# Kernel optimization log

Hardware: AMD Instinct MI355X
Metric: run time of the kernel (lower is better)

The kernel has to match this reference:

```python
import jax, jax.numpy as jnp
import numpy as np

N = 200000   # active voxels
K = 27       # 3x3x3 kernel volume
CIN = 32
COUT = 64


def setup_inputs() -> dict:
    key = jax.random.key(0)
    k1, k2, k3, k4 = jax.random.split(key, 4)
    features = jax.random.normal(k1, (N, CIN), dtype=jnp.float32)
    # kernel map: for each kernel offset k and output voxel n, index of the
    # contributing input voxel (or masked out if that neighbor is inactive)
    neighbor_map = jax.random.randint(k2, (K, N), 0, N, dtype=jnp.int32)
    neighbor_mask = jax.random.randint(k3, (K, N), 0, 2) > 0
    std = 1.0 / float(np.sqrt(CIN * K))  # matches reset_parameters
    kernel = jax.random.uniform(k4, (K, CIN, COUT), dtype=jnp.float32,
                                minval=-std, maxval=std)
    return {"features": features, "neighbor_map": neighbor_map,
            "neighbor_mask": neighbor_mask, "kernel": kernel}


def reference(features, neighbor_map, neighbor_mask, kernel):
    # Sparse conv3d as gather -> per-offset matmul -> accumulate.
    # scan over the K=27 kernel offsets keeps peak memory at one gathered
    # [N, CIN] buffer instead of materializing [K, N, CIN].
    n_out = features.shape[0]
    cout = kernel.shape[-1]

    def body(acc, inp):
        nm_k, mask_k, w_k = inp  # [N], [N], [CIN, COUT]
        g = features[nm_k] * mask_k[:, None].astype(features.dtype)  # gather [N, CIN]
        return acc + g @ w_k, None

    init = jnp.zeros((n_out, cout), dtype=features.dtype)
    out, _ = jax.lax.scan(body, init, (neighbor_map, neighbor_mask, kernel))
    return out
```

## Files before the change

### kernel.cpp

```cpp
#include <hip/hip_runtime.h>

#define CIN   32
#define COUT  64
#define K_OFF 27

typedef __attribute__((ext_vector_type(8))) short bf16x8;
typedef __attribute__((ext_vector_type(4))) float f32x4;

#define FENCE_VM(N) asm volatile("s_waitcnt vmcnt(" #N ")" ::: "memory")
#define PIN()       asm volatile("" ::: "memory")
#define BARRIER()   asm volatile("s_barrier" ::: "memory")

__device__ inline unsigned short f2bf_rne(float f) {
    union { float f; unsigned int u; } v; v.f = f;
    unsigned int u = v.u;
    u = (u + 0x7fffu + ((u >> 16) & 1u)) >> 16;
    return (unsigned short)u;
}

__device__ inline void async_load16(const void* g, void* l) {
    __builtin_amdgcn_global_load_lds(
        (const __attribute__((address_space(1))) void*)g,
        (__attribute__((address_space(3))) void*)l, 16, 0, 0);
}

__global__ __launch_bounds__(256) void prep_all(
    const float* __restrict__ feat, const int* __restrict__ nmap,
    const unsigned char* __restrict__ mask8, const float* __restrict__ wk,
    unsigned short* __restrict__ featb, int* __restrict__ midx,
    unsigned short* __restrict__ wt2, float* __restrict__ zrow,
    int n, int det_bytes)
{
    __shared__ int wany[4];
    const int tid = threadIdx.x;
    const int gsz = gridDim.x * 256;
    const int gt  = blockIdx.x * 256 + tid;

    {
        int found = 0;
        for (int i = tid; i < det_bytes; i += 256)
            if ((i & 3) && mask8[i]) found = 1;
        unsigned long long b = __ballot(found);
        if ((tid & 63) == 0) wany[tid >> 6] = b ? 1 : 0;
        __syncthreads();
    }
    const int is_b8 = wany[0] | wany[1] | wany[2] | wany[3];

    const int F = (n * CIN) / 8;
    for (int i = gt; i < F; i += gsz) {
        const int base = i * 8;
        float4 a = *(const float4*)(feat + base);
        float4 b = *(const float4*)(feat + base + 4);
        bf16x8 v;
        v[0] = (short)f2bf_rne(a.x); v[1] = (short)f2bf_rne(a.y);
        v[2] = (short)f2bf_rne(a.z); v[3] = (short)f2bf_rne(a.w);
        v[4] = (short)f2bf_rne(b.x); v[5] = (short)f2bf_rne(b.y);
        v[6] = (short)f2bf_rne(b.z); v[7] = (short)f2bf_rne(b.w);
        *(bf16x8*)(featb + base) = v;
    }

    {
        const int total = K_OFF * n;
        const int Q = (total + 3) / 4;
        for (int i = gt; i < Q; i += gsz) {
            int e = i * 4;
            if (e + 3 < total) {
                int4 nm = *(const int4*)(nmap + e);
                int m0, m1, m2, m3;
                if (is_b8) {
                    uchar4 mb = *(const uchar4*)(mask8 + e);
                    m0 = mb.x; m1 = mb.y; m2 = mb.z; m3 = mb.w;
                } else {
                    const int* m32 = (const int*)mask8;
                    int4 mm = *(const int4*)(m32 + e);
                    m0 = mm.x; m1 = mm.y; m2 = mm.z; m3 = mm.w;
                }
                int4 r;
                r.x = m0 ? nm.x : -1; r.y = m1 ? nm.y : -1;
                r.z = m2 ? nm.z : -1; r.w = m3 ? nm.w : -1;
                *(int4*)(midx + e) = r;
            } else {
                for (; e < total; ++e) {
                    int m = is_b8 ? (int)mask8[e] : ((const int*)mask8)[e];
                    midx[e] = m ? nmap[e] : -1;
                }
            }
        }
    }

    for (int t = gt; t < K_OFF * 4 * 64; t += gsz) {
        const int lane = t & 63, ct = (t >> 6) & 3, k = t >> 8;
        const int lrow = lane & 15, q = lane >> 4;
        const int col = ct * 16 + lrow;
        bf16x8 v;
        #pragma unroll
        for (int j = 0; j < 8; ++j)
            v[j] = (short)f2bf_rne(wk[(k * CIN + q * 8 + j) * COUT + col]);
        *(bf16x8*)(wt2 + t * 8) = v;
    }

    if (gt < 16) zrow[gt] = 0.0f;
}

__global__ __launch_bounds__(256) void conv_mfma10(
    const unsigned short* __restrict__ featb,
    const int*            __restrict__ midx,
    const unsigned short* __restrict__ wt2,
    const unsigned short* __restrict__ zrow,
    float* __restrict__ out, int n)
{
    __shared__ __attribute__((aligned(16))) unsigned short Bs[3][4][512];
    __shared__ __attribute__((aligned(16))) unsigned short As[3][4][2][512];

    const int tid  = threadIdx.x;
    const int wave = tid >> 6;
    const int lane = tid & 63;
    const int lrow = lane & 15;
    const int q    = lane >> 4;
    const int n0   = blockIdx.x * 128 + wave * 32;

    const int  row0 = n0 + lrow, row1 = n0 + 16 + lrow;
    const bool vr0 = row0 < n, vr1 = row1 < n;

    auto load_mi = [&](int k, int rt) -> int {
        const int  r = rt ? row1 : row0;
        const bool v = rt ? vr1 : vr0;
        if (!v) return -1;
        return midx[k * n + r];
    };
    auto issue_gather = [&](int mi, unsigned short* ldsbase) {
        const unsigned short* src =
            (mi >= 0) ? featb + (size_t)mi * CIN + q * 8 : zrow;
        async_load16(src, ldsbase);
    };
    auto stageB = [&](int k) {
        const unsigned short* src = wt2 + (((k * 4 + wave)) << 9) + lane * 8;
        async_load16(src, &Bs[k % 3][wave][0]);
    };

    int   mi_buf[2][2];
    f32x4 acc[2][4] = {};

    {
        int p00 = load_mi(0, 0), p01 = load_mi(0, 1);
        int p10 = load_mi(1, 0), p11 = load_mi(1, 1);
        mi_buf[0][0] = load_mi(2, 0); mi_buf[0][1] = load_mi(2, 1);
        mi_buf[1][0] = load_mi(3, 0); mi_buf[1][1] = load_mi(3, 1);
        PIN();
        stageB(0);
        stageB(1);
        PIN();
        issue_gather(p00, &As[0][wave][0][0]);
        issue_gather(p01, &As[0][wave][1][0]);
        PIN();
        issue_gather(p10, &As[1][wave][0][0]);
        issue_gather(p11, &As[1][wave][1][0]);
        PIN();
        FENCE_VM(2);
        BARRIER();
    }

    #pragma unroll
    for (int k = 0; k < K_OFF; ++k) {
        bf16x8 a0 = *(const bf16x8*)(&As[k % 3][wave][0][lane * 8]);
        bf16x8 a1 = *(const bf16x8*)(&As[k % 3][wave][1][lane * 8]);
        bf16x8 b0 = *(const bf16x8*)(&Bs[k % 3][0][lane * 8]);
        bf16x8 b1 = *(const bf16x8*)(&Bs[k % 3][1][lane * 8]);
        bf16x8 b2 = *(const bf16x8*)(&Bs[k % 3][2][lane * 8]);
        bf16x8 b3 = *(const bf16x8*)(&Bs[k % 3][3][lane * 8]);
        PIN();

        if (k + 2 < K_OFF) {
            stageB(k + 2);
            PIN();
            issue_gather(mi_buf[k & 1][0], &As[(k + 2) % 3][wave][0][0]);
            issue_gather(mi_buf[k & 1][1], &As[(k + 2) % 3][wave][1][0]);
            PIN();
        }
        if (k + 4 < K_OFF) {
            mi_buf[k & 1][0] = load_mi(k + 4, 0);
            mi_buf[k & 1][1] = load_mi(k + 4, 1);
            PIN();
        }

        acc[0][0] = __builtin_amdgcn_mfma_f32_16x16x32_bf16(a0, b0, acc[0][0], 0, 0, 0);
        acc[1][0] = __builtin_amdgcn_mfma_f32_16x16x32_bf16(a1, b0, acc[1][0], 0, 0, 0);
        acc[0][1] = __builtin_amdgcn_mfma_f32_16x16x32_bf16(a0, b1, acc[0][1], 0, 0, 0);
        acc[1][1] = __builtin_amdgcn_mfma_f32_16x16x32_bf16(a1, b1, acc[1][1], 0, 0, 0);
        acc[0][2] = __builtin_amdgcn_mfma_f32_16x16x32_bf16(a0, b2, acc[0][2], 0, 0, 0);
        acc[1][2] = __builtin_amdgcn_mfma_f32_16x16x32_bf16(a1, b2, acc[1][2], 0, 0, 0);
        acc[0][3] = __builtin_amdgcn_mfma_f32_16x16x32_bf16(a0, b3, acc[0][3], 0, 0, 0);
        acc[1][3] = __builtin_amdgcn_mfma_f32_16x16x32_bf16(a1, b3, acc[1][3], 0, 0, 0);

        if (k < K_OFF - 1) {
            if      (k == 0)  FENCE_VM(5);
            else if (k <= 22) FENCE_VM(7);
            else if (k == 23) FENCE_VM(5);
            else if (k == 24) FENCE_VM(3);
            else              FENCE_VM(0);
            BARRIER();
        }
    }

    #pragma unroll
    for (int rt = 0; rt < 2; ++rt)
        #pragma unroll
        for (int ct = 0; ct < 4; ++ct)
            #pragma unroll
            for (int r = 0; r < 4; ++r) {
                const int row = n0 + rt * 16 + q * 4 + r;
                if (row < n) out[(size_t)row * COUT + ct * 16 + lrow] = acc[rt][ct][r];
            }
}

__global__ __launch_bounds__(256) void detect_mask(
    const unsigned char* __restrict__ mask, int nbytes, int* __restrict__ flag,
    float* __restrict__ zrow) {
    __shared__ int wany[4];
    int found = 0;
    for (int i = threadIdx.x; i < nbytes; i += 256)
        if ((i & 3) && mask[i]) found = 1;
    unsigned long long b = __ballot(found);
    if ((threadIdx.x & 63) == 0) wany[threadIdx.x >> 6] = b ? 1 : 0;
    __syncthreads();
    if (threadIdx.x == 0) *flag = wany[0] | wany[1] | wany[2] | wany[3];
    if (threadIdx.x < 16) zrow[threadIdx.x] = 0.0f;
}

#define BN 64
__global__ __launch_bounds__(256) void sparse_conv_fp32(
    const float* __restrict__ feat, const int* __restrict__ nmap,
    const unsigned char* __restrict__ mask8, const int* __restrict__ mask32,
    const float* __restrict__ wk, float* __restrict__ out,
    int n, const int* __restrict__ flag)
{
    __shared__ float A[CIN][BN];
    __shared__ float W[CIN][COUT];
    const int tid = threadIdx.x;
    const int n0 = blockIdx.x * BN;
    const int is_b8 = *flag;
    const int r0 = (tid >> 4) * 4, c0 = (tid & 15) * 4;
    const int grow = tid >> 2, gpart = tid & 3;
    float acc[4][4] = {};
    for (int k = 0; k < K_OFF; ++k) {
        {
            const int base = tid * 8;
            const float* wsrc = wk + (size_t)k * (CIN * COUT) + base;
            float4 w0 = ((const float4*)wsrc)[0];
            float4 w1 = ((const float4*)wsrc)[1];
            *(float4*)&W[base >> 6][base & 63] = w0;
            *(float4*)&W[base >> 6][(base & 63) + 4] = w1;
        }
        {
            const int gn = n0 + grow;
            float4 f0 = make_float4(0.f, 0.f, 0.f, 0.f), f1 = f0;
            if (gn < n) {
                const int idx = k * n + gn;
                const int m = is_b8 ? (int)mask8[idx] : mask32[idx];
                if (m) {
                    const float* fsrc = feat + (size_t)nmap[idx] * CIN + gpart * 8;
                    f0 = ((const float4*)fsrc)[0];
                    f1 = ((const float4*)fsrc)[1];
                }
            }
            const int cb = gpart * 8;
            A[cb+0][grow]=f0.x; A[cb+1][grow]=f0.y; A[cb+2][grow]=f0.z; A[cb+3][grow]=f0.w;
            A[cb+4][grow]=f1.x; A[cb+5][grow]=f1.y; A[cb+6][grow]=f1.z; A[cb+7][grow]=f1.w;
        }
        __syncthreads();
        #pragma unroll
        for (int c = 0; c < CIN; ++c) {
            const float4 a = *(const float4*)&A[c][r0];
            const float4 w = *(const float4*)&W[c][c0];
            acc[0][0]+=a.x*w.x; acc[0][1]+=a.x*w.y; acc[0][2]+=a.x*w.z; acc[0][3]+=a.x*w.w;
            acc[1][0]+=a.y*w.x; acc[1][1]+=a.y*w.y; acc[1][2]+=a.y*w.z; acc[1][3]+=a.y*w.w;
            acc[2][0]+=a.z*w.x; acc[2][1]+=a.z*w.y; acc[2][2]+=a.z*w.z; acc[2][3]+=a.z*w.w;
            acc[3][0]+=a.w*w.x; acc[3][1]+=a.w*w.y; acc[3][2]+=a.w*w.z; acc[3][3]+=a.w*w.w;
        }
        __syncthreads();
    }
    #pragma unroll
    for (int i = 0; i < 4; ++i) {
        const int orow = n0 + r0 + i;
        if (orow < n)
            *(float4*)&out[(size_t)orow * COUT + c0] =
                make_float4(acc[i][0], acc[i][1], acc[i][2], acc[i][3]);
    }
}

static inline size_t align16(size_t x) { return (x + 15) & ~(size_t)15; }

extern "C" void kernel_launch(void* const* d_in, const int* in_sizes, int n_in,
                              void* d_out, int out_size, void* d_ws, size_t ws_size,
                              hipStream_t stream) {
    const float*         feat = (const float*)d_in[0];
    const int*           nmap = (const int*)d_in[1];
    const unsigned char* m8   = (const unsigned char*)d_in[2];
    const int*           m32  = (const int*)d_in[2];
    const float*         wk   = (const float*)d_in[3];
    float*               out  = (float*)d_out;

    const int n = in_sizes[0] / CIN;
    int*   flag = (int*)d_ws;
    float* zrow = (float*)((char*)d_ws + 64);

    const size_t feat_off   = 128;
    const size_t feat_bytes = (size_t)n * CIN * 2;
    const size_t midx_off   = align16(feat_off + feat_bytes);
    const size_t midx_bytes = (size_t)K_OFF * n * 4;
    const size_t wt2_off    = align16(midx_off + midx_bytes);
    const size_t wt2_bytes  = (size_t)K_OFF * 4 * 64 * 8 * 2;
    const size_t needed     = wt2_off + wt2_bytes;

    const int mask_elems = K_OFF * n;
    const int det_bytes  = mask_elems < 4096 ? mask_elems : 4096;

    if (ws_size >= needed) {
        unsigned short* featb = (unsigned short*)((char*)d_ws + feat_off);
        int*            midx  = (int*)((char*)d_ws + midx_off);
        unsigned short* wt2   = (unsigned short*)((char*)d_ws + wt2_off);

        prep_all<<<2048, 256, 0, stream>>>(
            feat, nmap, m8, wk, featb, midx, wt2, zrow, n, det_bytes);

        const int ntiles = (n + 127) / 128;
        conv_mfma10<<<ntiles, 256, 0, stream>>>(
            featb, midx, wt2, (const unsigned short*)zrow, out, n);
    } else {
        detect_mask<<<1, 256, 0, stream>>>(m8, det_bytes, flag, zrow);
        const int nb = (n + BN - 1) / BN;
        sparse_conv_fp32<<<nb, 256, 0, stream>>>(feat, nmap, m8, m32, wk, out, n, flag);
    }
}
```

Baseline: 168.6 us.

## Split 128-row tile across 8 waves with one 16-row strip each

The MFMA conv kernel now launches 512 threads per block, giving each of 8 waves a 16-row strip instead of 4 waves handling 32 rows each. Only the first four waves stage the weight tiles, and the per-wave vmcnt fences are split by role to match their differing outstanding load counts. The aim is more waves in flight, so more gather latency is hidden and per-wave register use drops. The cost is that each B fragment read from LDS now feeds half as many MFMAs, and barriers now synchronise twice as many waves.

```diff
diff --git a/kernel.cpp b/kernel.cpp
--- a/kernel.cpp
+++ b/kernel.cpp
@@ -102,7 +102,7 @@
     if (gt < 16) zrow[gt] = 0.0f;
 }
 
-__global__ __launch_bounds__(256) void conv_mfma10(
+__global__ __launch_bounds__(512) void conv_mfma16(
     const unsigned short* __restrict__ featb,
     const int*            __restrict__ midx,
     const unsigned short* __restrict__ wt2,
@@ -110,23 +110,22 @@
     float* __restrict__ out, int n)
 {
     __shared__ __attribute__((aligned(16))) unsigned short Bs[3][4][512];
-    __shared__ __attribute__((aligned(16))) unsigned short As[3][4][2][512];
+    __shared__ __attribute__((aligned(16))) unsigned short As[3][8][512];
 
     const int tid  = threadIdx.x;
     const int wave = tid >> 6;
     const int lane = tid & 63;
     const int lrow = lane & 15;
     const int q    = lane >> 4;
-    const int n0   = blockIdx.x * 128 + wave * 32;
-
-    const int  row0 = n0 + lrow, row1 = n0 + 16 + lrow;
-    const bool vr0 = row0 < n, vr1 = row1 < n;
-
-    auto load_mi = [&](int k, int rt) -> int {
-        const int  r = rt ? row1 : row0;
-        const bool v = rt ? vr1 : vr0;
-        if (!v) return -1;
-        return midx[k * n + r];
+    const int n0   = blockIdx.x * 128;
+    const int wr   = n0 + wave * 16;
+
+    const int  row  = wr + lrow;
+    const bool vrow = row < n;
+
+    auto load_mi = [&](int k) -> int {
+        if (!vrow) return -1;
+        return midx[k * n + row];
     };
     auto issue_gather = [&](int mi, unsigned short* ldsbase) {
         const unsigned short* src =
@@ -138,32 +137,26 @@
         async_load16(src, &Bs[k % 3][wave][0]);
     };
 
-    int   mi_buf[2][2];
-    f32x4 acc[2][4] = {};
+    int   mi_buf[2];
+    f32x4 acc[4] = {};
 
     {
-        int p00 = load_mi(0, 0), p01 = load_mi(0, 1);
-        int p10 = load_mi(1, 0), p11 = load_mi(1, 1);
-        mi_buf[0][0] = load_mi(2, 0); mi_buf[0][1] = load_mi(2, 1);
-        mi_buf[1][0] = load_mi(3, 0); mi_buf[1][1] = load_mi(3, 1);
-        PIN();
-        stageB(0);
-        stageB(1);
-        PIN();
-        issue_gather(p00, &As[0][wave][0][0]);
-        issue_gather(p01, &As[0][wave][1][0]);
-        PIN();
-        issue_gather(p10, &As[1][wave][0][0]);
-        issue_gather(p11, &As[1][wave][1][0]);
-        PIN();
-        FENCE_VM(2);
+        int p0 = load_mi(0), p1 = load_mi(1);
+        mi_buf[0] = load_mi(2); mi_buf[1] = load_mi(3);
+        PIN();
+        if (wave < 4) { stageB(0); stageB(1); }
+        PIN();
+        issue_gather(p0, &As[0][wave][0]);
+        PIN();
+        issue_gather(p1, &As[1][wave][0]);
+        PIN();
+        FENCE_VM(1);
         BARRIER();
     }
 
     #pragma unroll
     for (int k = 0; k < K_OFF; ++k) {
-        bf16x8 a0 = *(const bf16x8*)(&As[k % 3][wave][0][lane * 8]);
-        bf16x8 a1 = *(const bf16x8*)(&As[k % 3][wave][1][lane * 8]);
+        bf16x8 a0 = *(const bf16x8*)(&As[k % 3][wave][lane * 8]);
         bf16x8 b0 = *(const bf16x8*)(&Bs[k % 3][0][lane * 8]);
         bf16x8 b1 = *(const bf16x8*)(&Bs[k % 3][1][lane * 8]);
         bf16x8 b2 = *(const bf16x8*)(&Bs[k % 3][2][lane * 8]);
@@ -171,46 +164,46 @@
         PIN();
 
         if (k + 2 < K_OFF) {
-            stageB(k + 2);
+            if (wave < 4) { stageB(k + 2); }
             PIN();
-            issue_gather(mi_buf[k & 1][0], &As[(k + 2) % 3][wave][0][0]);
-            issue_gather(mi_buf[k & 1][1], &As[(k + 2) % 3][wave][1][0]);
+            issue_gather(mi_buf[k & 1], &As[(k + 2) % 3][wave][0]);
             PIN();
         }
         if (k + 4 < K_OFF) {
-            mi_buf[k & 1][0] = load_mi(k + 4, 0);
-            mi_buf[k & 1][1] = load_mi(k + 4, 1);
+            mi_buf[k & 1] = load_mi(k + 4);
             PIN();
         }
 
-        acc[0][0] = __builtin_amdgcn_mfma_f32_16x16x32_bf16(a0, b0, acc[0][0], 0, 0, 0);
-        acc[1][0] = __builtin_amdgcn_mfma_f32_16x16x32_bf16(a1, b0, acc[1][0], 0, 0, 0);
-        acc[0][1] = __builtin_amdgcn_mfma_f32_16x16x32_bf16(a0, b1, acc[0][1], 0, 0, 0);
-        acc[1][1] = __builtin_amdgcn_mfma_f32_16x16x32_bf16(a1, b1, acc[1][1], 0, 0, 0);
-        acc[0][2] = __builtin_amdgcn_mfma_f32_16x16x32_bf16(a0, b2, acc[0][2], 0, 0, 0);
-        acc[1][2] = __builtin_amdgcn_mfma_f32_16x16x32_bf16(a1, b2, acc[1][2], 0, 0, 0);
-        acc[0][3] = __builtin_amdgcn_mfma_f32_16x16x32_bf16(a0, b3, acc[0][3], 0, 0, 0);
-        acc[1][3] = __builtin_amdgcn_mfma_f32_16x16x32_bf16(a1, b3, acc[1][3], 0, 0, 0);
+        acc[0] = __builtin_amdgcn_mfma_f32_16x16x32_bf16(a0, b0, acc[0], 0, 0, 0);
+        acc[1] = __builtin_amdgcn_mfma_f32_16x16x32_bf16(a0, b1, acc[1], 0, 0, 0);
+        acc[2] = __builtin_amdgcn_mfma_f32_16x16x32_bf16(a0, b2, acc[2], 0, 0, 0);
+        acc[3] = __builtin_amdgcn_mfma_f32_16x16x32_bf16(a0, b3, acc[3], 0, 0, 0);
 
         if (k < K_OFF - 1) {
-            if      (k == 0)  FENCE_VM(5);
-            else if (k <= 22) FENCE_VM(7);
-            else if (k == 23) FENCE_VM(5);
-            else if (k == 24) FENCE_VM(3);
-            else              FENCE_VM(0);
+            if (wave < 4) {
+                if      (k == 0)  FENCE_VM(3);
+                else if (k <= 22) FENCE_VM(4);
+                else if (k == 23) FENCE_VM(3);
+                else if (k == 24) FENCE_VM(2);
+                else              FENCE_VM(0);
+            } else {
+                if      (k == 0)  FENCE_VM(2);
+                else if (k <= 22) FENCE_VM(3);
+                else if (k == 23) FENCE_VM(2);
+                else if (k == 24) FENCE_VM(1);
+                else              FENCE_VM(0);
+            }
             BARRIER();
         }
     }
 
     #pragma unroll
-    for (int rt = 0; rt < 2; ++rt)
+    for (int ct = 0; ct < 4; ++ct)
         #pragma unroll
-        for (int ct = 0; ct < 4; ++ct)
-            #pragma unroll
-            for (int r = 0; r < 4; ++r) {
-                const int row = n0 + rt * 16 + q * 4 + r;
-                if (row < n) out[(size_t)row * COUT + ct * 16 + lrow] = acc[rt][ct][r];
-            }
+        for (int r = 0; r < 4; ++r) {
+            const int orow = wr + q * 4 + r;
+            if (orow < n) out[(size_t)orow * COUT + ct * 16 + lrow] = acc[ct][r];
+        }
 }
 
 __global__ __launch_bounds__(256) void detect_mask(
@@ -324,7 +317,7 @@
             feat, nmap, m8, wk, featb, midx, wt2, zrow, n, det_bytes);
 
         const int ntiles = (n + 127) / 128;
-        conv_mfma10<<<ntiles, 256, 0, stream>>>(
+        conv_mfma16<<<ntiles, 512, 0, stream>>>(
             featb, midx, wt2, (const unsigned short*)zrow, out, n);
     } else {
         detect_mask<<<1, 256, 0, stream>>>(m8, det_bytes, flag, zrow);
```

Result: no change. 167.5 us (-0.7%).
